# Optimization experiments

Hardware: AMD Instinct MI355X
Metric: run time of the kernel (lower is better)

Reference implementation:

```python
import jax, jax.numpy as jnp
import numpy as np

DIM = 2048
N_HEADS = 16
QK_NOPE = 128
QK_ROPE = 64
V_DIM = 128
QK_DIM = QK_NOPE + QK_ROPE  # 192
B, S = 2, 2048


def setup_inputs() -> dict:
    key = jax.random.key(0)
    ks = jax.random.split(key, 6)
    x = jax.random.normal(ks[0], (B, S, DIM), dtype=jnp.float32)
    # rotary angles: theta[j] = 10000^{-2j/d}, angle[p, j] = p * theta[j]
    inv_freq = 1.0 / (10000.0 ** (np.arange(0, QK_ROPE, 2, dtype=np.float32) / QK_ROPE))
    freqs = jnp.asarray(np.arange(S, dtype=np.float32)[:, None] * inv_freq[None, :])  # [S, QK_ROPE//2]
    # additive causal mask
    mask = jnp.where(jnp.tril(jnp.ones((S, S), dtype=bool)), 0.0, -1e9).astype(jnp.float32)
    sc = 1.0 / np.sqrt(DIM)
    wq = jax.random.normal(ks[1], (DIM, N_HEADS * QK_DIM), dtype=jnp.float32) * sc
    wk = jax.random.normal(ks[2], (DIM, N_HEADS * QK_DIM), dtype=jnp.float32) * sc
    wv = jax.random.normal(ks[3], (DIM, N_HEADS * V_DIM), dtype=jnp.float32) * sc
    wo = jax.random.normal(ks[4], (N_HEADS * V_DIM, DIM), dtype=jnp.float32) * (1.0 / np.sqrt(N_HEADS * V_DIM))
    return {"x": x, "start_pos": 0, "freqs": freqs, "mask": mask,
            "wq": wq, "wk": wk, "wv": wv, "wo": wo}


def _apply_rope(t, freqs):
    # t: [B, S, H, D_rope]; freqs: [S, D_rope//2] angles
    b, s, h, d = t.shape
    tr = t.reshape(b, s, h, d // 2, 2)
    cos = jnp.cos(freqs)[None, :, None, :]
    sin = jnp.sin(freqs)[None, :, None, :]
    out = jnp.stack([tr[..., 0] * cos - tr[..., 1] * sin,
                     tr[..., 0] * sin + tr[..., 1] * cos], axis=-1)
    return out.reshape(b, s, h, d)


def reference(x, start_pos, freqs, mask, wq, wk, wv, wo):
    b, s, _ = x.shape
    xq = x @ wq  # [B,S,H*QK_DIM]
    xk = x @ wk
    xv = (x @ wv).reshape(b, s, N_HEADS, V_DIM)
    qnope, qrope = jnp.split(xq, [N_HEADS * QK_NOPE], axis=-1)
    knope, krope = jnp.split(xk, [N_HEADS * QK_NOPE], axis=-1)
    qnope = qnope.reshape(b, s, N_HEADS, QK_NOPE)
    knope = knope.reshape(b, s, N_HEADS, QK_NOPE)
    qrope = _apply_rope(qrope.reshape(b, s, N_HEADS, QK_ROPE), freqs)
    krope = _apply_rope(krope.reshape(b, s, N_HEADS, QK_ROPE), freqs)
    q = jnp.concatenate([qnope, qrope], axis=-1)  # [B,S,H,QK_DIM]
    k = jnp.concatenate([knope, krope], axis=-1)
    scale = 1.0 / jnp.sqrt(jnp.asarray(QK_DIM, dtype=q.dtype))
    scores = jnp.einsum('bqhd,bkhd->bhqk', q, k) * scale
    scores = scores + mask[None, None, :, :]
    attn = jax.nn.softmax(scores.astype(jnp.float32), axis=-1).astype(scores.dtype)
    out = jnp.einsum('bhqk,bkhd->bqhd', attn, xv)  # [B,S,H,V_DIM]
    out = out.reshape(b, s, N_HEADS * V_DIM)
    return out @ wo
```

## Files before the change

### kernel.cpp

```cpp
#include <hip/hip_runtime.h>
#include <hip/hip_bf16.h>

typedef __attribute__((ext_vector_type(4))) float f32x4;
typedef __attribute__((ext_vector_type(8))) short s16x8;
typedef unsigned int u32;
typedef unsigned short u16;

#define GLDS16(gp, lp) __builtin_amdgcn_global_load_lds(                         \
    (const __attribute__((address_space(1))) u32*)(gp),                          \
    (__attribute__((address_space(3))) u32*)(lp), 16, 0, 0)
#define VMCNT10 asm volatile("s_waitcnt vmcnt(10)" ::: "memory")
#define VMCNT6 asm volatile("s_waitcnt vmcnt(6)" ::: "memory")
#define VMCNT4 asm volatile("s_waitcnt vmcnt(4)" ::: "memory")
#define VMCNT0 asm volatile("s_waitcnt vmcnt(0)" ::: "memory")
#define LGKM8  asm volatile("s_waitcnt lgkmcnt(8)" ::: "memory")
#define LGKM0  asm volatile("s_waitcnt lgkmcnt(0)" ::: "memory")
#define SBAR   __builtin_amdgcn_sched_barrier(0)

__device__ __forceinline__ u16 f2bf(float f) {
    u32 u = __builtin_bit_cast(u32, f);
    u32 r = (u + 0x7FFFu + ((u >> 16) & 1u)) >> 16;
    return (u16)r;
}
__device__ __forceinline__ float bf2f(u16 h) {
    u32 u = ((u32)h) << 16;
    return __builtin_bit_cast(float, u);
}

__global__ __launch_bounds__(256) void prep(const float4* __restrict__ x,
                                            ushort4* __restrict__ xb4,
                                            const float* __restrict__ wq,
                                            const float* __restrict__ wk,
                                            const float* __restrict__ wv,
                                            const float* __restrict__ wo,
                                            u16* __restrict__ WT,
                                            u16* __restrict__ woT) {
    __shared__ float tile[32][33];
    int bid = blockIdx.x;
    if (bid < 8192) {
        int i = bid * 256 + threadIdx.x;
        float4 v = x[i];
        ushort4 o;
        o.x = f2bf(v.x); o.y = f2bf(v.y); o.z = f2bf(v.z); o.w = f2bf(v.w);
        xb4[i] = o;
        return;
    }
    bid -= 8192;
    const float* src;
    u16* dst;
    int N, bx, by;
    if (bid < 6144)       { src = wq; dst = WT;                        N = 3072; bx = bid % 96; by = bid / 96; }
    else if (bid < 12288) { bid -= 6144;  src = wk; dst = WT + (size_t)3072 * 2048; N = 3072; bx = bid % 96; by = bid / 96; }
    else if (bid < 16384) { bid -= 12288; src = wv; dst = WT + (size_t)6144 * 2048; N = 2048; bx = bid % 64; by = bid / 64; }
    else                  { bid -= 16384; src = wo; dst = woT;         N = 2048; bx = bid % 64; by = bid / 64; }
    int n0 = bx * 32, k0 = by * 32;
    int tx = threadIdx.x & 31, ty = threadIdx.x >> 5;
#pragma unroll
    for (int i = 0; i < 4; ++i)
        tile[ty + i * 8][tx] = src[(size_t)(k0 + ty + i * 8) * N + n0 + tx];
    __syncthreads();
#pragma unroll
    for (int i = 0; i < 4; ++i) {
        int n = ty + i * 8;
        dst[(size_t)(n0 + n) * 2048 + k0 + tx] = f2bf(tile[tx][n]);
    }
}

__global__ __launch_bounds__(512, 2) void gemm_qkv(const u16* __restrict__ A,
                                                   const u16* __restrict__ W,
                                                   u16* __restrict__ Qh,
                                                   u16* __restrict__ Kh,
                                                   u16* __restrict__ Vn) {
    __shared__ __align__(16) u16 S[2][2][2][128 * 64];
    const int tid = threadIdx.x, lane = tid & 63, wid = tid >> 6;
    const int l15 = lane & 15, l4 = lane >> 4;
    const int id = blockIdx.x;
    const int nt = ((id & 7) << 2) + ((id >> 3) & 3);
    const int mt = id >> 5;
    const int bm0 = mt << 8, bn0 = nt << 8;
    const int wr = wid >> 2, wc = wid & 3;
    f32x4 acc[8][4] = {};

    auto stageH = [&](int mat, int tt, int h) {
        const int kc = tt << 6, p = tt & 1;
        const u16* G = mat ? W : A;
        const int rbase = (mat ? bn0 : bm0) + (h << 7);
        u16* Ld = S[mat][p][h];
#pragma unroll
        for (int j = 0; j < 2; ++j) {
            int c = j * 512 + tid;
            int row = c >> 3, ch = c & 7;
            int cs = ch ^ (row & 7);
            GLDS16(G + (size_t)(rbase + row) * 2048 + kc + cs * 8,
                   (char*)Ld + (j * 512 + wid * 64) * 16);
        }
    };

    s16x8 af[2][2], bfr[4][2];

#define RDA(P, I)                                                              \
    _Pragma("unroll") for (int mm = 0; mm < 2; ++mm)                           \
    _Pragma("unroll") for (int kk = 0; kk < 2; ++kk) {                         \
        int r7 = ((I) * 2 + mm) * 16 + l15;                                    \
        int byt = r7 * 128 + (((kk * 4 + l4) ^ (r7 & 7)) << 4);                \
        af[mm][kk] = *(const s16x8*)((const char*)S[0][P][wr] + byt);          \
    }
#define RDB(P)                                                                 \
    _Pragma("unroll") for (int n = 0; n < 4; ++n)                              \
    _Pragma("unroll") for (int kk = 0; kk < 2; ++kk) {                         \
        int r7 = (wc & 1) * 64 + n * 16 + l15;                                 \
        int byt = r7 * 128 + (((kk * 4 + l4) ^ (r7 & 7)) << 4);                \
        bfr[n][kk] = *(const s16x8*)((const char*)S[1][P][wc >> 1] + byt);     \
    }
#define MF(I)                                                                  \
    __builtin_amdgcn_s_setprio(1);                                             \
    _Pragma("unroll") for (int mm = 0; mm < 2; ++mm)                           \
    _Pragma("unroll") for (int n = 0; n < 4; ++n)                              \
    _Pragma("unroll") for (int kk = 0; kk < 2; ++kk)                           \
        acc[(I) * 2 + mm][n] = __builtin_amdgcn_mfma_f32_16x16x32_bf16(        \
            af[mm][kk], bfr[n][kk], acc[(I) * 2 + mm][n], 0, 0, 0);            \
    __builtin_amdgcn_s_setprio(0);

    stageH(0, 0, 0); stageH(0, 0, 1); stageH(1, 0, 0); stageH(1, 0, 1);
    stageH(0, 1, 0); stageH(0, 1, 1);
    VMCNT4;
    __builtin_amdgcn_s_barrier();
    SBAR;

    for (int t = 0; t < 32; ++t) {
        const int p = t & 1;
        RDB(p); RDA(p, 0);
        if (t == 0) stageH(1, 1, 0);
        else if (t < 31) stageH(0, t + 1, 0);
        LGKM8; SBAR;
        __builtin_amdgcn_s_barrier();
        LGKM0; SBAR;
        MF(0); SBAR;
        __builtin_amdgcn_s_barrier();
        RDA(p, 1);
        if (t == 0) stageH(1, 1, 1);
        else if (t < 31) stageH(0, t + 1, 1);
        __builtin_amdgcn_s_barrier();
        LGKM0; SBAR;
        MF(1); SBAR;
        __builtin_amdgcn_s_barrier();
        RDA(p, 2);
        if (t < 30) stageH(1, t + 2, 0);
        __builtin_amdgcn_s_barrier();
        LGKM0; SBAR;
        MF(2); SBAR;
        __builtin_amdgcn_s_barrier();
        RDA(p, 3);
        if (t < 30) stageH(1, t + 2, 1);
        __builtin_amdgcn_s_barrier();
        LGKM0; SBAR;
        MF(3); SBAR;
        if (t < 31) {
            if (t < 30) { VMCNT4; } else { VMCNT0; }
            SBAR;
        }
        __builtin_amdgcn_s_barrier();
    }
#undef RDA
#undef RDB
#undef MF

#pragma unroll
    for (int m = 0; m < 8; ++m)
#pragma unroll
        for (int n = 0; n < 4; ++n)
#pragma unroll
            for (int r = 0; r < 4; ++r) {
                int row = bm0 + wr * 128 + m * 16 + l4 * 4 + r;
                int c = bn0 + wc * 64 + n * 16 + l15;
                float v = acc[m][n][r];
                if (bn0 >= 6144) {
                    Vn[(size_t)row * 2048 + (c - 6144)] = f2bf(v);
                } else {
                    u16* dst = (bn0 >= 3072) ? Kh : Qh;
                    int cc = (bn0 >= 3072) ? c - 3072 : c;
                    int b = row >> 11, s = row & 2047;
                    int h, d;
                    if (cc < 2048) { h = cc >> 7; d = cc & 127; }
                    else { int mm = cc - 2048; h = mm >> 6; d = 128 + (mm & 63); }
                    dst[(((size_t)b * 16 + h) * 2048 + s) * 192 + d] = f2bf(v);
                }
            }
}

__global__ __launch_bounds__(256) void gemm_bt_f32(const u16* __restrict__ A,
                                                   const u16* __restrict__ Bt,
                                                   float* __restrict__ C,
                                                   int M, int N, int K) {
    __shared__ __align__(16) u16 As[128 * 64];
    __shared__ __align__(16) u16 Bs[128 * 64];
    const int tid = threadIdx.x, lane = tid & 63, wid = tid >> 6;
    const int l15 = lane & 15, l4 = lane >> 4;
    const int bm0 = blockIdx.y << 7, bn0 = blockIdx.x << 7;
    const int wr = wid >> 1, wc = wid & 1;
    f32x4 acc[4][4] = {};
    const int nk = K >> 6;
    for (int t = 0; t < nk; ++t) {
        const int k0 = t << 6;
#pragma unroll
        for (int i = 0; i < 4; ++i) {
            int c = i * 256 + tid;
            int row = c >> 3, c8 = c & 7;
            GLDS16(A + (size_t)(bm0 + row) * K + k0 + c8 * 8,
                   (char*)As + (i * 256 + wid * 64) * 16);
        }
#pragma unroll
        for (int i = 0; i < 4; ++i) {
            int c = i * 256 + tid;
            int row = c >> 3, c8 = c & 7;
            GLDS16(Bt + (size_t)(bn0 + row) * K + k0 + c8 * 8,
                   (char*)Bs + (i * 256 + wid * 64) * 16);
        }
        __syncthreads();
#pragma unroll
        for (int kk = 0; kk < 64; kk += 32) {
            s16x8 af[4], bfr[4];
#pragma unroll
            for (int m = 0; m < 4; ++m)
                af[m] = *(const s16x8*)(As + (wr * 64 + m * 16 + l15) * 64 + kk + l4 * 8);
#pragma unroll
            for (int n = 0; n < 4; ++n)
                bfr[n] = *(const s16x8*)(Bs + (wc * 64 + n * 16 + l15) * 64 + kk + l4 * 8);
#pragma unroll
            for (int m = 0; m < 4; ++m)
#pragma unroll
                for (int n = 0; n < 4; ++n)
                    acc[m][n] = __builtin_amdgcn_mfma_f32_16x16x32_bf16(af[m], bfr[n],
                                                                        acc[m][n], 0, 0, 0);
        }
        __syncthreads();
    }
#pragma unroll
    for (int m = 0; m < 4; ++m)
#pragma unroll
        for (int n = 0; n < 4; ++n)
#pragma unroll
            for (int r = 0; r < 4; ++r) {
                int row = bm0 + wr * 64 + m * 16 + l4 * 4 + r;
                int col = bn0 + wc * 64 + n * 16 + l15;
                C[(size_t)row * N + col] = acc[m][n][r];
            }
}

__global__ __launch_bounds__(256) void rope_inplace(u16* __restrict__ T,
                                                    const float* __restrict__ freqs) {
    int idx = blockIdx.x * 256 + threadIdx.x;
    int j = idx & 31, s = (idx >> 5) & 2047, bh = idx >> 16;
    float ang = freqs[s * 32 + j];
    float c = cosf(ang), sn = sinf(ang);
    u32* p = (u32*)(T + ((size_t)bh * 2048 + s) * 192 + 128) + j;
    u32 v = *p;
    float t0 = bf2f((u16)(v & 0xffff)), t1 = bf2f((u16)(v >> 16));
    float o0 = t0 * c - t1 * sn;
    float o1 = t0 * sn + t1 * c;
    *p = (u32)f2bf(o0) | ((u32)f2bf(o1) << 16);
}

__global__ __launch_bounds__(256) void vtrans(const u16* __restrict__ Vn,
                                              u16* __restrict__ Vt) {
    __shared__ u16 tile[32][33];
    int s0 = blockIdx.x * 32, d0 = blockIdx.y * 32, bh = blockIdx.z;
    int b = bh >> 4, h = bh & 15;
    int tx = threadIdx.x & 31, ty = threadIdx.x >> 5;
#pragma unroll
    for (int i = 0; i < 4; ++i) {
        int s = ty + i * 8;
        tile[s][tx] = Vn[((size_t)b * 2048 + s0 + s) * 2048 + h * 128 + d0 + tx];
    }
    __syncthreads();
#pragma unroll
    for (int i = 0; i < 4; ++i) {
        int d = ty + i * 8;
        Vt[((size_t)bh * 128 + d0 + d) * 2048 + s0 + tx] = tile[tx][d];
    }
}

__global__ __launch_bounds__(256) void attn_fwd3(const u16* __restrict__ Qh,
                                                 const u16* __restrict__ Kh,
                                                 const u16* __restrict__ Vt,
                                                 u16* __restrict__ AO) {
    __shared__ __align__(16) u16 Ks[2][64 * 192];
    __shared__ __align__(16) u16 Vs[128 * 64];
    __shared__ __align__(16) u16 Ps[4][32 * 64];
    const int tid = threadIdx.x, lane = tid & 63, wid = tid >> 6;
    const int l15 = lane & 15, l4 = lane >> 4;
    const int id = blockIdx.x;
    const int bh = id & 31;
    const int qt = 15 - (id >> 5);
    const int q0 = qt << 7;
    const u16* Qb = Qh + ((size_t)bh * 2048 + q0 + wid * 32) * 192;
    const u16* Kb = Kh + (size_t)bh * 2048 * 192;
    const u16* Vb = Vt + (size_t)bh * 128 * 2048;

    auto stageK = [&](int t, int buf) {
        const int k0 = t << 6;
#pragma unroll
        for (int i = 0; i < 6; ++i) {
            int c = i * 256 + tid;
            int row = (u32)c / 24u, cc = c - row * 24;
            int cs = (cc & 24) | ((cc ^ row) & 7);
            GLDS16(Kb + (size_t)(k0 + row) * 192 + cs * 8,
                   (char*)Ks[buf] + (i * 256 + wid * 64) * 16);
        }
    };
    auto stageV = [&](int t) {
        const int k0 = t << 6;
#pragma unroll
        for (int i = 0; i < 4; ++i) {
            int c = i * 256 + tid;
            int d = c >> 3, cc = c & 7;
            int cs = cc ^ (d & 7);
            GLDS16(Vb + (size_t)d * 2048 + k0 + cs * 8,
                   (char*)Vs + (i * 256 + wid * 64) * 16);
        }
    };

    s16x8 aq[2][6];
#pragma unroll
    for (int qg = 0; qg < 2; ++qg)
#pragma unroll
        for (int dk = 0; dk < 6; ++dk)
            aq[qg][dk] = *(const s16x8*)(Qb + (size_t)(qg * 16 + l15) * 192 + dk * 32 + l4 * 8);

    f32x4 acc[2][8] = {};
    float mrow[2][4], lpart[2][4];
#pragma unroll
    for (int qg = 0; qg < 2; ++qg)
#pragma unroll
        for (int r = 0; r < 4; ++r) { mrow[qg][r] = -1e30f; lpart[qg][r] = 0.f; }
    const float scale = 0.07216878364870322f;

    const int ntile = (qt + 1) << 1;
    stageK(0, 0);
    for (int t = 0; t < ntile; ++t) {
        const int cur = t & 1;
        const int k0 = t << 6;
        const bool pf = (t + 1 < ntile);
        stageV(t);
        if (pf) stageK(t + 1, cur ^ 1);
        if (pf) { VMCNT10; } else { VMCNT4; }
        SBAR;
        __builtin_amdgcn_s_barrier();
        SBAR;

        const bool live = (q0 + wid * 32 + 31 >= k0);
        if (live) {
            const u16* Kc = Ks[cur];
            f32x4 sc[2][4];
#pragma unroll
            for (int qg = 0; qg < 2; ++qg)
#pragma unroll
                for (int kg = 0; kg < 4; ++kg) sc[qg][kg] = f32x4{0.f, 0.f, 0.f, 0.f};
            __builtin_amdgcn_s_setprio(1);
#pragma unroll
            for (int dk = 0; dk < 6; ++dk) {
                s16x8 bk[4];
#pragma unroll
                for (int kg = 0; kg < 4; ++kg) {
                    int row = kg * 16 + l15;
                    int byt = (row * 384 + dk * 64 + l4 * 16) ^ ((row & 7) << 4);
                    bk[kg] = *(const s16x8*)((const char*)Kc + byt);
                }
#pragma unroll
                for (int qg = 0; qg < 2; ++qg)
#pragma unroll
                    for (int kg = 0; kg < 4; ++kg)
                        sc[qg][kg] = __builtin_amdgcn_mfma_f32_16x16x32_bf16(
                            aq[qg][dk], bk[kg], sc[qg][kg], 0, 0, 0);
            }
            __builtin_amdgcn_s_setprio(0);

            u16* Pw = Ps[wid];
#pragma unroll
            for (int qg = 0; qg < 2; ++qg) {
                const int qrow = q0 + wid * 32 + qg * 16 + l4 * 4;
                const bool domask = (k0 + 63 > qrow);
                float p[4][4], tm[4];
#pragma unroll
                for (int r = 0; r < 4; ++r) tm[r] = -1e30f;
#pragma unroll
                for (int kg = 0; kg < 4; ++kg)
#pragma unroll
                    for (int r = 0; r < 4; ++r) {
                        float v = sc[qg][kg][r] * scale;
                        if (domask && (k0 + kg * 16 + l15 > qrow + r)) v = -1e30f;
                        p[kg][r] = v;
                        tm[r] = fmaxf(tm[r], v);
                    }
#pragma unroll
                for (int off = 1; off < 16; off <<= 1)
#pragma unroll
                    for (int r = 0; r < 4; ++r)
                        tm[r] = fmaxf(tm[r], __shfl_xor(tm[r], off, 64));
                float mn[4];
                bool resc = false;
#pragma unroll
                for (int r = 0; r < 4; ++r) {
                    mn[r] = (tm[r] <= mrow[qg][r] + 8.f) ? mrow[qg][r] : tm[r];
                    resc |= (mn[r] > mrow[qg][r]);
                }
                if (__any(resc)) {
#pragma unroll
                    for (int r = 0; r < 4; ++r) {
                        float scl = __expf(mrow[qg][r] - mn[r]);
                        mrow[qg][r] = mn[r];
                        lpart[qg][r] *= scl;
#pragma unroll
                        for (int db = 0; db < 8; ++db) acc[qg][db][r] *= scl;
                    }
                }
#pragma unroll
                for (int kg = 0; kg < 4; ++kg)
#pragma unroll
                    for (int r = 0; r < 4; ++r) {
                        p[kg][r] = __expf(p[kg][r] - mrow[qg][r]);
                        lpart[qg][r] += p[kg][r];
                    }
#pragma unroll
                for (int kg = 0; kg < 4; ++kg)
#pragma unroll
                    for (int r = 0; r < 4; ++r) {
                        int row = qg * 16 + l4 * 4 + r;
                        int byt = ((row * 64 + kg * 16 + l15) * 2) ^ ((row & 7) << 4);
                        *(u16*)((char*)Pw + byt) = f2bf(p[kg][r]);
                    }
            }
        }

        if (pf) { VMCNT6; } else { VMCNT0; }
        SBAR;
        __builtin_amdgcn_s_barrier();
        SBAR;

        if (live) {
            u16* Pw = Ps[wid];
            __builtin_amdgcn_s_setprio(1);
#pragma unroll
            for (int kk = 0; kk < 2; ++kk) {
                s16x8 ap[2];
#pragma unroll
                for (int qg = 0; qg < 2; ++qg) {
                    int row = qg * 16 + l15;
                    int byt = ((row * 64 + kk * 32 + l4 * 8) * 2) ^ ((row & 7) << 4);
                    ap[qg] = *(const s16x8*)((const char*)Pw + byt);
                }
#pragma unroll
                for (int db = 0; db < 8; ++db) {
                    int row = db * 16 + l15;
                    int byt = (row * 128 + kk * 64 + l4 * 16) ^ ((row & 7) << 4);
                    s16x8 bv = *(const s16x8*)((const char*)Vs + byt);
#pragma unroll
                    for (int qg = 0; qg < 2; ++qg)
                        acc[qg][db] = __builtin_amdgcn_mfma_f32_16x16x32_bf16(
                            ap[qg], bv, acc[qg][db], 0, 0, 0);
                }
            }
            __builtin_amdgcn_s_setprio(0);
        }
        SBAR;
        __builtin_amdgcn_s_barrier();
        SBAR;
    }

#pragma unroll
    for (int off = 1; off < 16; off <<= 1)
#pragma unroll
        for (int qg = 0; qg < 2; ++qg)
#pragma unroll
            for (int r = 0; r < 4; ++r)
                lpart[qg][r] += __shfl_xor(lpart[qg][r], off, 64);

    const int b = bh >> 4, h = bh & 15;
#pragma unroll
    for (int qg = 0; qg < 2; ++qg) {
        float inv[4];
#pragma unroll
        for (int r = 0; r < 4; ++r) inv[r] = 1.f / lpart[qg][r];
#pragma unroll
        for (int db = 0; db < 8; ++db)
#pragma unroll
            for (int r = 0; r < 4; ++r) {
                int row = q0 + wid * 32 + qg * 16 + l4 * 4 + r;
                AO[((size_t)b * 2048 + row) * 2048 + h * 128 + db * 16 + l15] =
                    f2bf(acc[qg][db][r] * inv[r]);
            }
    }
}

extern "C" void kernel_launch(void* const* d_in, const int* in_sizes, int n_in,
                              void* d_out, int out_size, void* d_ws, size_t ws_size,
                              hipStream_t stream) {
    const float* x     = (const float*)d_in[0];
    const float* freqs = (const float*)d_in[2];
    const float* wq    = (const float*)d_in[4];
    const float* wk    = (const float*)d_in[5];
    const float* wv    = (const float*)d_in[6];
    const float* wo    = (const float*)d_in[7];
    float* out = (float*)d_out;

    char* ws = (char*)d_ws;
    u16* xb   = (u16*)(ws + 0);
    u16* WT   = (u16*)(ws + 16777216);
    u16* woT  = (u16*)(ws + 50331648);
    u16* Qh   = (u16*)(ws + 58720256);
    u16* Kh   = (u16*)(ws + 83886080);
    u16* Vn   = (u16*)(ws + 109051904);
    u16* Vt   = (u16*)(ws + 125829120);
    u16* AO   = (u16*)(ws + 142606336);

    prep<<<28672, 256, 0, stream>>>((const float4*)x, (ushort4*)xb,
                                    wq, wk, wv, wo, WT, woT);
    gemm_qkv<<<dim3(512), 512, 0, stream>>>(xb, WT, Qh, Kh, Vn);
    rope_inplace<<<8192, 256, 0, stream>>>(Qh, freqs);
    rope_inplace<<<8192, 256, 0, stream>>>(Kh, freqs);
    vtrans<<<dim3(64, 4, 32), 256, 0, stream>>>(Vn, Vt);
    attn_fwd3<<<dim3(512), 256, 0, stream>>>(Qh, Kh, Vt, AO);
    gemm_bt_f32<<<dim3(16, 32), 256, 0, stream>>>(AO, woT, out, 4096, 2048, 2048);
}
```

Before: 349.2 us.

## Widen weight transpose tiles, merge RoPE launches, reorder attention tile schedule

```diff
diff --git a/kernel.cpp b/kernel.cpp
--- a/kernel.cpp
+++ b/kernel.cpp
@@ -35,7 +35,7 @@
                                             const float* __restrict__ wo,
                                             u16* __restrict__ WT,
                                             u16* __restrict__ woT) {
-    __shared__ float tile[32][33];
+    __shared__ float tile[32][132];
     int bid = blockIdx.x;
     if (bid < 8192) {
         int i = bid * 256 + threadIdx.x;
@@ -49,20 +49,27 @@
     const float* src;
     u16* dst;
     int N, bx, by;
-    if (bid < 6144)       { src = wq; dst = WT;                        N = 3072; bx = bid % 96; by = bid / 96; }
-    else if (bid < 12288) { bid -= 6144;  src = wk; dst = WT + (size_t)3072 * 2048; N = 3072; bx = bid % 96; by = bid / 96; }
-    else if (bid < 16384) { bid -= 12288; src = wv; dst = WT + (size_t)6144 * 2048; N = 2048; bx = bid % 64; by = bid / 64; }
-    else                  { bid -= 16384; src = wo; dst = woT;         N = 2048; bx = bid % 64; by = bid / 64; }
-    int n0 = bx * 32, k0 = by * 32;
-    int tx = threadIdx.x & 31, ty = threadIdx.x >> 5;
-#pragma unroll
-    for (int i = 0; i < 4; ++i)
-        tile[ty + i * 8][tx] = src[(size_t)(k0 + ty + i * 8) * N + n0 + tx];
+    if (bid < 1536)      { src = wq; dst = WT;                         N = 3072; bx = bid % 24; by = bid / 24; }
+    else if (bid < 3072) { bid -= 1536; src = wk; dst = WT + (size_t)3072 * 2048; N = 3072; bx = bid % 24; by = bid / 24; }
+    else if (bid < 4096) { bid -= 3072; src = wv; dst = WT + (size_t)6144 * 2048; N = 2048; bx = bid % 16; by = bid / 16; }
+    else                 { bid -= 4096; src = wo; dst = woT;           N = 2048; bx = bid % 16; by = bid / 16; }
+    int n0 = bx * 128, k0 = by * 32;
+    int nf = threadIdx.x & 31, kr = threadIdx.x >> 5;
+#pragma unroll
+    for (int i = 0; i < 4; ++i) {
+        int row = kr + i * 8;
+        float4 v = *(const float4*)&src[(size_t)(k0 + row) * N + n0 + 4 * nf];
+        tile[row][4 * nf + 0] = v.x;
+        tile[row][4 * nf + 1] = v.y;
+        tile[row][4 * nf + 2] = v.z;
+        tile[row][4 * nf + 3] = v.w;
+    }
     __syncthreads();
-#pragma unroll
-    for (int i = 0; i < 4; ++i) {
-        int n = ty + i * 8;
-        dst[(size_t)(n0 + n) * 2048 + k0 + tx] = f2bf(tile[tx][n]);
+    int kk = threadIdx.x & 31, nr0 = threadIdx.x >> 5;
+#pragma unroll
+    for (int i = 0; i < 16; ++i) {
+        int n = nr0 + i * 8;
+        dst[(size_t)(n0 + n) * 2048 + k0 + kk] = f2bf(tile[kk][n]);
     }
 }
 
@@ -247,10 +254,13 @@
             }
 }
 
-__global__ __launch_bounds__(256) void rope_inplace(u16* __restrict__ T,
-                                                    const float* __restrict__ freqs) {
+__global__ __launch_bounds__(256) void rope2(u16* __restrict__ Qh,
+                                             u16* __restrict__ Kh,
+                                             const float* __restrict__ freqs) {
     int idx = blockIdx.x * 256 + threadIdx.x;
-    int j = idx & 31, s = (idx >> 5) & 2047, bh = idx >> 16;
+    int j = idx & 31, s = (idx >> 5) & 2047, u = idx >> 16;
+    u16* T = (u < 32) ? Qh : Kh;
+    int bh = u & 31;
     float ang = freqs[s * 32 + j];
     float c = cosf(ang), sn = sinf(ang);
     u32* p = (u32*)(T + ((size_t)bh * 2048 + s) * 192 + 128) + j;
@@ -291,7 +301,8 @@
     const int l15 = lane & 15, l4 = lane >> 4;
     const int id = blockIdx.x;
     const int bh = id & 31;
-    const int qt = 15 - (id >> 5);
+    const int j = (id & 255) >> 5;
+    const int qt = (id < 256) ? (15 - j) : j;
     const int q0 = qt << 7;
     const u16* Qb = Qh + ((size_t)bh * 2048 + q0 + wid * 32) * 192;
     const u16* Kb = Kh + (size_t)bh * 2048 * 192;
@@ -513,11 +524,10 @@
     u16* Vt   = (u16*)(ws + 125829120);
     u16* AO   = (u16*)(ws + 142606336);
 
-    prep<<<28672, 256, 0, stream>>>((const float4*)x, (ushort4*)xb,
+    prep<<<13312, 256, 0, stream>>>((const float4*)x, (ushort4*)xb,
                                     wq, wk, wv, wo, WT, woT);
     gemm_qkv<<<dim3(512), 512, 0, stream>>>(xb, WT, Qh, Kh, Vn);
-    rope_inplace<<<8192, 256, 0, stream>>>(Qh, freqs);
-    rope_inplace<<<8192, 256, 0, stream>>>(Kh, freqs);
+    rope2<<<16384, 256, 0, stream>>>(Qh, Kh, freqs);
     vtrans<<<dim3(64, 4, 32), 256, 0, stream>>>(Vn, Vt);
     attn_fwd3<<<dim3(512), 256, 0, stream>>>(Qh, Kh, Vt, AO);
     gemm_bt_f32<<<dim3(16, 32), 256, 0, stream>>>(AO, woT, out, 4096, 2048, 2048);
```

Result: slower. 383.3 us (+9.8%).
